# Kernel tuning notes

Hardware: AMD Instinct MI355X
Metric: run time of the kernel (lower is better)

The kernel has to match this reference:

```python
import jax, jax.numpy as jnp
import numpy as np

N_ATOMS = 200000
AEV_DIM = 384
H1, H2, H3 = 160, 128, 96
N_SPECIES = 4
ALPHA = 0.1  # CELU alpha used by ANI atomic networks


def setup_inputs() -> dict:
    key = jax.random.key(0)
    ks = jax.random.split(key, 8)
    aev = jax.random.normal(ks[0], (N_ATOMS, AEV_DIM), dtype=jnp.float32)
    # Disjoint species partition (matches (species==s).nonzero() buffers)
    perm = jax.random.permutation(ks[1], N_ATOMS)
    chunk = N_ATOMS // N_SPECIES
    H_idx = perm[0 * chunk:1 * chunk]
    C_idx = perm[1 * chunk:2 * chunk]
    N_idx = perm[2 * chunk:3 * chunk]
    O_idx = perm[3 * chunk:4 * chunk]

    def init(k, shape, fan_in):
        return (jax.random.normal(k, shape, dtype=jnp.float32) / np.float32(np.sqrt(fan_in)))

    # Stacked per-species MLP params: leading axis = species (H,C,N,O)
    W1 = init(ks[2], (N_SPECIES, AEV_DIM, H1), AEV_DIM); b1 = jnp.zeros((N_SPECIES, H1), jnp.float32)
    W2 = init(ks[3], (N_SPECIES, H1, H2), H1);          b2 = jnp.zeros((N_SPECIES, H2), jnp.float32)
    W3 = init(ks[4], (N_SPECIES, H2, H3), H2);          b3 = jnp.zeros((N_SPECIES, H3), jnp.float32)
    W4 = init(ks[5], (N_SPECIES, H3, 1), H3);           b4 = jnp.zeros((N_SPECIES, 1), jnp.float32)
    return {"aev": aev,
            "W1": W1, "b1": b1, "W2": W2, "b2": b2,
            "W3": W3, "b3": b3, "W4": W4, "b4": b4,
            "H_idx": H_idx, "C_idx": C_idx, "N_idx": N_idx, "O_idx": O_idx}


def _species_mlp(x, W1, b1, W2, b2, W3, b3, W4, b4):
    h = jax.nn.celu(x @ W1 + b1, ALPHA)
    h = jax.nn.celu(h @ W2 + b2, ALPHA)
    h = jax.nn.celu(h @ W3 + b3, ALPHA)
    return (h @ W4 + b4).reshape(-1)  # per-atom scalar energy


def reference(aev, W1, b1, W2, b2, W3, b3, W4, b4, H_idx, C_idx, N_idx, O_idx):
    out = jnp.zeros((aev.shape[0],), dtype=aev.dtype)
    # Fixed small loop over the 4 species networks (structurally distinct experts)
    for s, idx in enumerate((H_idx, C_idx, N_idx, O_idx)):
        e = _species_mlp(aev[idx], W1[s], b1[s], W2[s], b2[s], W3[s], b3[s], W4[s], b4[s])
        out = out.at[idx].add(e)  # index_add_ scatter
    # output.unsqueeze(0).sum(dim=1) -> molecular energy, shape [1]
    return out[None, :].sum(axis=1)
```

## Files before the change

### kernel.cpp

```cpp
#include <hip/hip_runtime.h>

#define DI __device__ __forceinline__

constexpr int AEV = 384;
constexpr int H1N = 160;
constexpr int H2N = 128;
constexpr int H3N = 96;
constexpr int NSP = 4;
constexpr int TM  = 128;
constexpr int SP1 = 168;
constexpr int SP2 = 136;
constexpr int SP3 = 104;

using half8  = __attribute__((ext_vector_type(8))) _Float16;
using half4v = __attribute__((ext_vector_type(4))) _Float16;
using f32x4  = __attribute__((ext_vector_type(4))) float;

__device__ __align__(16) _Float16 g_w1[NSP * H1N * AEV];
__device__ __align__(16) _Float16 g_w2[NSP * H2N * H1N];
__device__ __align__(16) _Float16 g_w3[NSP * H3N * H2N];

DI float celu_f(float x) {
  return fmaxf(x, 0.f) + 0.1f * (exp2f(fminf(x, 0.f) * 14.426950408889634f) - 1.f);
}
DI f32x4 mfma16h(half8 a, half8 b, f32x4 c) {
  return __builtin_amdgcn_mfma_f32_16x16x32_f16(a, b, c, 0, 0, 0);
}
DI half8 cvt8(float4 a, float4 b) {
  half8 t;
  t[0] = (_Float16)a.x; t[1] = (_Float16)a.y; t[2] = (_Float16)a.z; t[3] = (_Float16)a.w;
  t[4] = (_Float16)b.x; t[5] = (_Float16)b.y; t[6] = (_Float16)b.z; t[7] = (_Float16)b.w;
  return t;
}

template <int K, int N>
DI void tp(const float* __restrict__ src, _Float16* dst, int id) {
  constexpr int per = K * N;
  int s = id / per, r = id % per;
  int n = r / K, k = r % K;
  dst[s * per + n * K + k] = (_Float16)src[s * per + k * N + n];
}

__global__ void prep(const float* __restrict__ W1, const float* __restrict__ W2,
                     const float* __restrict__ W3, float* __restrict__ out) {
  int id = blockIdx.x * 256 + threadIdx.x;
  if (id == 0) out[0] = 0.f;
  constexpr int E1 = NSP * AEV * H1N;
  constexpr int E2 = NSP * H1N * H2N;
  constexpr int E3 = NSP * H2N * H3N;
  if (id < E1)                 tp<AEV, H1N>(W1, g_w1, id);
  else if (id < E1 + E2)       tp<H1N, H2N>(W2, g_w2, id - E1);
  else if (id < E1 + E2 + E3)  tp<H2N, H3N>(W3, g_w3, id - E1 - E2);
}

__global__ void __launch_bounds__(256) __attribute__((amdgpu_waves_per_eu(2, 2)))
fused_mlp(const float* __restrict__ aev,
          const float* __restrict__ b1, const float* __restrict__ b2,
          const float* __restrict__ b3,
          const float* __restrict__ W4, const float* __restrict__ pb4,
          const int* __restrict__ i0, const int* __restrict__ i1,
          const int* __restrict__ i2, const int* __restrict__ i3,
          int chunk, float* __restrict__ out) {
  __shared__ __align__(16) _Float16 HB[4 * 32 * (SP1 + SP2)];
  __shared__ float RED[4];

  const int tid  = threadIdx.x;
  const int lane = tid & 63, wav = tid >> 6;
  const int l15  = lane & 15, quad = lane >> 4;
  const int s    = blockIdx.y;
  const int* idx = (s == 0) ? i0 : (s == 1) ? i1 : (s == 2) ? i2 : i3;

  _Float16* H1w = HB + wav * (32 * SP1);
  _Float16* H2w = HB + 4 * (32 * SP1) + wav * (32 * SP2);

  const _Float16* w1 = g_w1 + s * H1N * AEV;
  const _Float16* w2 = g_w2 + s * H2N * H1N;
  const _Float16* w3 = g_w3 + s * H3N * H2N;

  const int abase = (blockIdx.x * 4 + wav) * 32;
  const int a0 = abase + l15, a1 = a0 + 16;
  const int r0 = idx[a0 < chunk ? a0 : (chunk - 1)];
  const int r1 = idx[a1 < chunk ? a1 : (chunk - 1)];
  const float* xr0 = aev + (size_t)r0 * AEV + quad * 8;
  const float* xr1 = aev + (size_t)r1 * AEV + quad * 8;

  f32x4 acc[10][2];
#pragma unroll
  for (int m = 0; m < 10; ++m)
#pragma unroll
    for (int nt = 0; nt < 2; ++nt)
#pragma unroll
      for (int i = 0; i < 4; ++i) acc[m][nt][i] = 0.f;

  float4 xf00, xf01, xf10, xf11;
  xf00 = *(const float4*)(xr0); xf01 = *(const float4*)(xr0 + 4);
  xf10 = *(const float4*)(xr1); xf11 = *(const float4*)(xr1 + 4);

#pragma unroll
  for (int ks = 0; ks < 12; ++ks) {
    half8 bv0 = cvt8(xf00, xf01);
    half8 bv1 = cvt8(xf10, xf11);
    if (ks < 11) {
      xf00 = *(const float4*)(xr0 + (ks + 1) * 32);
      xf01 = *(const float4*)(xr0 + (ks + 1) * 32 + 4);
      xf10 = *(const float4*)(xr1 + (ks + 1) * 32);
      xf11 = *(const float4*)(xr1 + (ks + 1) * 32 + 4);
    }
    const _Float16* pa = w1 + l15 * AEV + ks * 32 + quad * 8;
#pragma unroll
    for (int mt = 0; mt < 10; ++mt) {
      half8 a = *(const half8*)(pa + mt * 16 * AEV);
      acc[mt][0] = mfma16h(a, bv0, acc[mt][0]);
      acc[mt][1] = mfma16h(a, bv1, acc[mt][1]);
    }
  }
#pragma unroll
  for (int mt = 0; mt < 10; ++mt) {
    float4 bb = *(const float4*)(b1 + s * H1N + mt * 16 + quad * 4);
#pragma unroll
    for (int nt = 0; nt < 2; ++nt) {
      int atom = nt * 16 + l15;
      half4v o;
      o[0] = (_Float16)celu_f(acc[mt][nt][0] + bb.x);
      o[1] = (_Float16)celu_f(acc[mt][nt][1] + bb.y);
      o[2] = (_Float16)celu_f(acc[mt][nt][2] + bb.z);
      o[3] = (_Float16)celu_f(acc[mt][nt][3] + bb.w);
      *(half4v*)(H1w + atom * SP1 + mt * 16 + quad * 4) = o;
    }
  }

  {
    f32x4 acc2[8][2];
#pragma unroll
    for (int m = 0; m < 8; ++m)
#pragma unroll
      for (int nt = 0; nt < 2; ++nt)
#pragma unroll
        for (int i = 0; i < 4; ++i) acc2[m][nt][i] = 0.f;
    half8 bb2[5][2];
#pragma unroll
    for (int ks = 0; ks < 5; ++ks)
#pragma unroll
      for (int nt = 0; nt < 2; ++nt)
        bb2[ks][nt] = *(const half8*)(H1w + (nt * 16 + l15) * SP1 + ks * 32 + quad * 8);
#pragma unroll
    for (int mt = 0; mt < 8; ++mt) {
      const _Float16* pa = w2 + (mt * 16 + l15) * H1N + quad * 8;
#pragma unroll
      for (int ks = 0; ks < 5; ++ks) {
        half8 a = *(const half8*)(pa + ks * 32);
        acc2[mt][0] = mfma16h(a, bb2[ks][0], acc2[mt][0]);
        acc2[mt][1] = mfma16h(a, bb2[ks][1], acc2[mt][1]);
      }
    }
#pragma unroll
    for (int mt = 0; mt < 8; ++mt) {
      float4 bb = *(const float4*)(b2 + s * H2N + mt * 16 + quad * 4);
#pragma unroll
      for (int nt = 0; nt < 2; ++nt) {
        int atom = nt * 16 + l15;
        half4v o;
        o[0] = (_Float16)celu_f(acc2[mt][nt][0] + bb.x);
        o[1] = (_Float16)celu_f(acc2[mt][nt][1] + bb.y);
        o[2] = (_Float16)celu_f(acc2[mt][nt][2] + bb.z);
        o[3] = (_Float16)celu_f(acc2[mt][nt][3] + bb.w);
        *(half4v*)(H2w + atom * SP2 + mt * 16 + quad * 4) = o;
      }
    }
  }

  {
    f32x4 acc3[6][2];
#pragma unroll
    for (int m = 0; m < 6; ++m)
#pragma unroll
      for (int nt = 0; nt < 2; ++nt)
#pragma unroll
        for (int i = 0; i < 4; ++i) acc3[m][nt][i] = 0.f;
    half8 bb3[4][2];
#pragma unroll
    for (int ks = 0; ks < 4; ++ks)
#pragma unroll
      for (int nt = 0; nt < 2; ++nt)
        bb3[ks][nt] = *(const half8*)(H2w + (nt * 16 + l15) * SP2 + ks * 32 + quad * 8);
#pragma unroll
    for (int mt = 0; mt < 6; ++mt) {
      const _Float16* pa = w3 + (mt * 16 + l15) * H2N + quad * 8;
#pragma unroll
      for (int ks = 0; ks < 4; ++ks) {
        half8 a = *(const half8*)(pa + ks * 32);
        acc3[mt][0] = mfma16h(a, bb3[ks][0], acc3[mt][0]);
        acc3[mt][1] = mfma16h(a, bb3[ks][1], acc3[mt][1]);
      }
    }
#pragma unroll
    for (int mt = 0; mt < 6; ++mt) {
      float4 bb = *(const float4*)(b3 + s * H3N + mt * 16 + quad * 4);
#pragma unroll
      for (int nt = 0; nt < 2; ++nt) {
        int atom = nt * 16 + l15;
        half4v o;
        o[0] = (_Float16)celu_f(acc3[mt][nt][0] + bb.x);
        o[1] = (_Float16)celu_f(acc3[mt][nt][1] + bb.y);
        o[2] = (_Float16)celu_f(acc3[mt][nt][2] + bb.z);
        o[3] = (_Float16)celu_f(acc3[mt][nt][3] + bb.w);
        *(half4v*)(H1w + atom * SP3 + mt * 16 + quad * 4) = o;
      }
    }
  }

  {
    const int atom = lane >> 1, h = lane & 1;
    const _Float16* h3 = H1w + atom * SP3 + h * 48;
    const float* w4 = W4 + s * H3N + h * 48;
    float e = 0.f;
#pragma unroll
    for (int j = 0; j < 6; ++j) {
      half8 hv = *(const half8*)(h3 + j * 8);
      float4 wa = *(const float4*)(w4 + j * 8);
      float4 wb = *(const float4*)(w4 + j * 8 + 4);
      e += (float)hv[0] * wa.x + (float)hv[1] * wa.y + (float)hv[2] * wa.z + (float)hv[3] * wa.w
         + (float)hv[4] * wb.x + (float)hv[5] * wb.y + (float)hv[6] * wb.z + (float)hv[7] * wb.w;
    }
    e += __shfl_down(e, 1, 64);
    bool valid = (h == 0) && (abase + atom < chunk);
    e = valid ? (e + pb4[s]) : 0.f;
#pragma unroll
    for (int off = 32; off > 0; off >>= 1) e += __shfl_down(e, off, 64);
    if (lane == 0) RED[wav] = e;
  }
  __syncthreads();
  if (tid == 0) atomicAdd(out, RED[0] + RED[1] + RED[2] + RED[3]);
}

extern "C" void kernel_launch(void* const* d_in, const int* in_sizes, int n_in,
                              void* d_out, int out_size, void* d_ws, size_t ws_size,
                              hipStream_t stream) {
  (void)n_in; (void)d_ws; (void)ws_size; (void)out_size;
  const float* aev = (const float*)d_in[0];
  const float* W1  = (const float*)d_in[1];
  const float* b1  = (const float*)d_in[2];
  const float* W2  = (const float*)d_in[3];
  const float* b2  = (const float*)d_in[4];
  const float* W3  = (const float*)d_in[5];
  const float* b3  = (const float*)d_in[6];
  const float* W4  = (const float*)d_in[7];
  const float* b4  = (const float*)d_in[8];
  const int* iH = (const int*)d_in[9];
  const int* iC = (const int*)d_in[10];
  const int* iN = (const int*)d_in[11];
  const int* iO = (const int*)d_in[12];
  const int chunk = in_sizes[9];

  constexpr int TOT = NSP * (AEV * H1N + H1N * H2N + H2N * H3N);
  prep<<<TOT / 256, 256, 0, stream>>>(W1, W2, W3, (float*)d_out);

  const int tiles = (chunk + TM - 1) / TM;
  dim3 grid(tiles, NSP);
  fused_mlp<<<grid, 256, 0, stream>>>(aev, b1, b2, b3, W4, b4,
                                      iH, iC, iN, iO, chunk, (float*)d_out);
}
```

Measured before the change: 582.6 us.

## Split fused MLP into layer-1 and layers-2-4 kernels with LDS-resident weights

Replaces the single fused kernel with two kernels. The first computes layer 1 from gathered AEV rows using W1 staged in shared memory and writes fp16 hidden activations to a global buffer. The second stages W2 and W3 in shared memory and runs layers 2–4 plus the reduction. The aim is to stop re-reading weight fragments from global memory for every tile, which costs an extra global round trip for the H1 activations, large LDS footprints, and 1024-thread blocks that may limit occupancy.

```diff
diff --git a/kernel.cpp b/kernel.cpp
--- a/kernel.cpp
+++ b/kernel.cpp
@@ -7,10 +7,10 @@
 constexpr int H2N = 128;
 constexpr int H3N = 96;
 constexpr int NSP = 4;
-constexpr int TM  = 128;
-constexpr int SP1 = 168;
-constexpr int SP2 = 136;
-constexpr int SP3 = 104;
+constexpr int W1P = 392;
+constexpr int W2P = 168;
+constexpr int W3P = 136;
+constexpr int NMAX = 200000;
 
 using half8  = __attribute__((ext_vector_type(8))) _Float16;
 using half4v = __attribute__((ext_vector_type(4))) _Float16;
@@ -19,6 +19,7 @@
 __device__ __align__(16) _Float16 g_w1[NSP * H1N * AEV];
 __device__ __align__(16) _Float16 g_w2[NSP * H2N * H1N];
 __device__ __align__(16) _Float16 g_w3[NSP * H3N * H2N];
+__device__ __align__(16) _Float16 g_h1[(size_t)NMAX * H1N];
 
 DI float celu_f(float x) {
   return fmaxf(x, 0.f) + 0.1f * (exp2f(fminf(x, 0.f) * 14.426950408889634f) - 1.f);
@@ -53,16 +54,12 @@
   else if (id < E1 + E2 + E3)  tp<H2N, H3N>(W3, g_w3, id - E1 - E2);
 }
 
-__global__ void __launch_bounds__(256) __attribute__((amdgpu_waves_per_eu(2, 2)))
-fused_mlp(const float* __restrict__ aev,
-          const float* __restrict__ b1, const float* __restrict__ b2,
-          const float* __restrict__ b3,
-          const float* __restrict__ W4, const float* __restrict__ pb4,
-          const int* __restrict__ i0, const int* __restrict__ i1,
-          const int* __restrict__ i2, const int* __restrict__ i3,
-          int chunk, float* __restrict__ out) {
-  __shared__ __align__(16) _Float16 HB[4 * 32 * (SP1 + SP2)];
-  __shared__ float RED[4];
+__global__ __launch_bounds__(1024, 4) void layer1_k(
+    const float* __restrict__ aev, const float* __restrict__ b1,
+    const int* __restrict__ i0, const int* __restrict__ i1,
+    const int* __restrict__ i2, const int* __restrict__ i3,
+    int chunk) {
+  __shared__ __align__(16) _Float16 W1s[H1N * W1P];
 
   const int tid  = threadIdx.x;
   const int lane = tid & 63, wav = tid >> 6;
@@ -70,167 +67,174 @@
   const int s    = blockIdx.y;
   const int* idx = (s == 0) ? i0 : (s == 1) ? i1 : (s == 2) ? i2 : i3;
 
-  _Float16* H1w = HB + wav * (32 * SP1);
-  _Float16* H2w = HB + 4 * (32 * SP1) + wav * (32 * SP2);
-
-  const _Float16* w1 = g_w1 + s * H1N * AEV;
-  const _Float16* w2 = g_w2 + s * H2N * H1N;
-  const _Float16* w3 = g_w3 + s * H3N * H2N;
-
-  const int abase = (blockIdx.x * 4 + wav) * 32;
-  const int a0 = abase + l15, a1 = a0 + 16;
-  const int r0 = idx[a0 < chunk ? a0 : (chunk - 1)];
-  const int r1 = idx[a1 < chunk ? a1 : (chunk - 1)];
-  const float* xr0 = aev + (size_t)r0 * AEV + quad * 8;
-  const float* xr1 = aev + (size_t)r1 * AEV + quad * 8;
-
-  f32x4 acc[10][2];
+  const _Float16* wsrc = g_w1 + (size_t)s * H1N * AEV;
+#pragma unroll
+  for (int i = 0; i < 8; ++i) {
+    int c = tid + i * 1024;
+    if (c < H1N * (AEV / 8)) {
+      int n = c / (AEV / 8), kc = c % (AEV / 8);
+      *(half8*)(W1s + n * W1P + kc * 8) = *(const half8*)(wsrc + n * AEV + kc * 8);
+    }
+  }
+  __syncthreads();
+
+  const int a = blockIdx.x * 256 + wav * 16 + l15;
+  const bool valid = (a < chunk);
+  const int r = idx[valid ? a : (chunk - 1)];
+  const float* xr = aev + (size_t)r * AEV + quad * 8;
+
+  f32x4 acc[10];
 #pragma unroll
   for (int m = 0; m < 10; ++m)
 #pragma unroll
-    for (int nt = 0; nt < 2; ++nt)
-#pragma unroll
-      for (int i = 0; i < 4; ++i) acc[m][nt][i] = 0.f;
-
-  float4 xf00, xf01, xf10, xf11;
-  xf00 = *(const float4*)(xr0); xf01 = *(const float4*)(xr0 + 4);
-  xf10 = *(const float4*)(xr1); xf11 = *(const float4*)(xr1 + 4);
-
+    for (int i = 0; i < 4; ++i) acc[m][i] = 0.f;
+
+  float4 xf0 = *(const float4*)(xr), xf1 = *(const float4*)(xr + 4);
 #pragma unroll
   for (int ks = 0; ks < 12; ++ks) {
-    half8 bv0 = cvt8(xf00, xf01);
-    half8 bv1 = cvt8(xf10, xf11);
+    half8 bv = cvt8(xf0, xf1);
     if (ks < 11) {
-      xf00 = *(const float4*)(xr0 + (ks + 1) * 32);
-      xf01 = *(const float4*)(xr0 + (ks + 1) * 32 + 4);
-      xf10 = *(const float4*)(xr1 + (ks + 1) * 32);
-      xf11 = *(const float4*)(xr1 + (ks + 1) * 32 + 4);
-    }
-    const _Float16* pa = w1 + l15 * AEV + ks * 32 + quad * 8;
+      xf0 = *(const float4*)(xr + (ks + 1) * 32);
+      xf1 = *(const float4*)(xr + (ks + 1) * 32 + 4);
+    }
 #pragma unroll
     for (int mt = 0; mt < 10; ++mt) {
-      half8 a = *(const half8*)(pa + mt * 16 * AEV);
-      acc[mt][0] = mfma16h(a, bv0, acc[mt][0]);
-      acc[mt][1] = mfma16h(a, bv1, acc[mt][1]);
-    }
-  }
+      half8 aw = *(const half8*)(W1s + (mt * 16 + l15) * W1P + ks * 32 + quad * 8);
+      acc[mt] = mfma16h(aw, bv, acc[mt]);
+    }
+  }
+  _Float16* hrow = g_h1 + ((size_t)s * chunk + a) * H1N;
 #pragma unroll
   for (int mt = 0; mt < 10; ++mt) {
     float4 bb = *(const float4*)(b1 + s * H1N + mt * 16 + quad * 4);
-#pragma unroll
-    for (int nt = 0; nt < 2; ++nt) {
-      int atom = nt * 16 + l15;
-      half4v o;
-      o[0] = (_Float16)celu_f(acc[mt][nt][0] + bb.x);
-      o[1] = (_Float16)celu_f(acc[mt][nt][1] + bb.y);
-      o[2] = (_Float16)celu_f(acc[mt][nt][2] + bb.z);
-      o[3] = (_Float16)celu_f(acc[mt][nt][3] + bb.w);
-      *(half4v*)(H1w + atom * SP1 + mt * 16 + quad * 4) = o;
-    }
-  }
-
+    half4v o;
+    o[0] = (_Float16)celu_f(acc[mt][0] + bb.x);
+    o[1] = (_Float16)celu_f(acc[mt][1] + bb.y);
+    o[2] = (_Float16)celu_f(acc[mt][2] + bb.z);
+    o[3] = (_Float16)celu_f(acc[mt][3] + bb.w);
+    if (valid) *(half4v*)(hrow + mt * 16 + quad * 4) = o;
+  }
+}
+
+__global__ __launch_bounds__(1024, 4) void layer234_k(
+    const float* __restrict__ b2, const float* __restrict__ b3,
+    const float* __restrict__ W4, const float* __restrict__ pb4,
+    int chunk, float* __restrict__ out) {
+  __shared__ __align__(16) _Float16 W2s[H2N * W2P];
+  __shared__ __align__(16) _Float16 W3s[H3N * W3P];
+  __shared__ __align__(16) _Float16 H2s[16 * 16 * W3P];
+  __shared__ float RED[16];
+
+  const int tid  = threadIdx.x;
+  const int lane = tid & 63, wav = tid >> 6;
+  const int l15  = lane & 15, quad = lane >> 4;
+  const int s    = blockIdx.y;
+
+  const _Float16* w2src = g_w2 + (size_t)s * H2N * H1N;
+  const _Float16* w3src = g_w3 + (size_t)s * H3N * H2N;
+#pragma unroll
+  for (int i = 0; i < 3; ++i) {
+    int c = tid + i * 1024;
+    if (c < H2N * (H1N / 8)) {
+      int n = c / (H1N / 8), kc = c % (H1N / 8);
+      *(half8*)(W2s + n * W2P + kc * 8) = *(const half8*)(w2src + n * H1N + kc * 8);
+    }
+  }
+#pragma unroll
+  for (int i = 0; i < 2; ++i) {
+    int c = tid + i * 1024;
+    if (c < H3N * (H2N / 8)) {
+      int n = c / (H2N / 8), kc = c % (H2N / 8);
+      *(half8*)(W3s + n * W3P + kc * 8) = *(const half8*)(w3src + n * H2N + kc * 8);
+    }
+  }
+  __syncthreads();
+
+  const int a = blockIdx.x * 256 + wav * 16 + l15;
+  const bool valid = (a < chunk);
+  const int ac = valid ? a : (chunk - 1);
+  const _Float16* hrow = g_h1 + ((size_t)s * chunk + ac) * H1N + quad * 8;
+  _Float16* H2w = H2s + wav * (16 * W3P);
+
+  half8 bv2[5];
+#pragma unroll
+  for (int ks = 0; ks < 5; ++ks) bv2[ks] = *(const half8*)(hrow + ks * 32);
+  f32x4 acc2[8];
+#pragma unroll
+  for (int m = 0; m < 8; ++m)
+#pragma unroll
+    for (int i = 0; i < 4; ++i) acc2[m][i] = 0.f;
+#pragma unroll
+  for (int mt = 0; mt < 8; ++mt)
+#pragma unroll
+    for (int ks = 0; ks < 5; ++ks) {
+      half8 aw = *(const half8*)(W2s + (mt * 16 + l15) * W2P + ks * 32 + quad * 8);
+      acc2[mt] = mfma16h(aw, bv2[ks], acc2[mt]);
+    }
+#pragma unroll
+  for (int mt = 0; mt < 8; ++mt) {
+    float4 bb = *(const float4*)(b2 + s * H2N + mt * 16 + quad * 4);
+    half4v o;
+    o[0] = (_Float16)celu_f(acc2[mt][0] + bb.x);
+    o[1] = (_Float16)celu_f(acc2[mt][1] + bb.y);
+    o[2] = (_Float16)celu_f(acc2[mt][2] + bb.z);
+    o[3] = (_Float16)celu_f(acc2[mt][3] + bb.w);
+    *(half4v*)(H2w + l15 * W3P + mt * 16 + quad * 4) = o;
+  }
+
+  half8 bv3[4];
+#pragma unroll
+  for (int ks = 0; ks < 4; ++ks)
+    bv3[ks] = *(const half8*)(H2w + l15 * W3P + ks * 32 + quad * 8);
+  f32x4 acc3[6];
+#pragma unroll
+  for (int m = 0; m < 6; ++m)
+#pragma unroll
+    for (int i = 0; i < 4; ++i) acc3[m][i] = 0.f;
+#pragma unroll
+  for (int mt = 0; mt < 6; ++mt)
+#pragma unroll
+    for (int ks = 0; ks < 4; ++ks) {
+      half8 aw = *(const half8*)(W3s + (mt * 16 + l15) * W3P + ks * 32 + quad * 8);
+      acc3[mt] = mfma16h(aw, bv3[ks], acc3[mt]);
+    }
+#pragma unroll
+  for (int mt = 0; mt < 6; ++mt) {
+    float4 bb = *(const float4*)(b3 + s * H3N + mt * 16 + quad * 4);
+    half4v o;
+    o[0] = (_Float16)celu_f(acc3[mt][0] + bb.x);
+    o[1] = (_Float16)celu_f(acc3[mt][1] + bb.y);
+    o[2] = (_Float16)celu_f(acc3[mt][2] + bb.z);
+    o[3] = (_Float16)celu_f(acc3[mt][3] + bb.w);
+    *(half4v*)(H2w + l15 * W3P + mt * 16 + quad * 4) = o;
+  }
+
+  float e = 0.f;
   {
-    f32x4 acc2[8][2];
-#pragma unroll
-    for (int m = 0; m < 8; ++m)
-#pragma unroll
-      for (int nt = 0; nt < 2; ++nt)
-#pragma unroll
-        for (int i = 0; i < 4; ++i) acc2[m][nt][i] = 0.f;
-    half8 bb2[5][2];
-#pragma unroll
-    for (int ks = 0; ks < 5; ++ks)
-#pragma unroll
-      for (int nt = 0; nt < 2; ++nt)
-        bb2[ks][nt] = *(const half8*)(H1w + (nt * 16 + l15) * SP1 + ks * 32 + quad * 8);
-#pragma unroll
-    for (int mt = 0; mt < 8; ++mt) {
-      const _Float16* pa = w2 + (mt * 16 + l15) * H1N + quad * 8;
-#pragma unroll
-      for (int ks = 0; ks < 5; ++ks) {
-        half8 a = *(const half8*)(pa + ks * 32);
-        acc2[mt][0] = mfma16h(a, bb2[ks][0], acc2[mt][0]);
-        acc2[mt][1] = mfma16h(a, bb2[ks][1], acc2[mt][1]);
-      }
-    }
-#pragma unroll
-    for (int mt = 0; mt < 8; ++mt) {
-      float4 bb = *(const float4*)(b2 + s * H2N + mt * 16 + quad * 4);
-#pragma unroll
-      for (int nt = 0; nt < 2; ++nt) {
-        int atom = nt * 16 + l15;
-        half4v o;
-        o[0] = (_Float16)celu_f(acc2[mt][nt][0] + bb.x);
-        o[1] = (_Float16)celu_f(acc2[mt][nt][1] + bb.y);
-        o[2] = (_Float16)celu_f(acc2[mt][nt][2] + bb.z);
-        o[3] = (_Float16)celu_f(acc2[mt][nt][3] + bb.w);
-        *(half4v*)(H2w + atom * SP2 + mt * 16 + quad * 4) = o;
-      }
-    }
-  }
-
-  {
-    f32x4 acc3[6][2];
-#pragma unroll
-    for (int m = 0; m < 6; ++m)
-#pragma unroll
-      for (int nt = 0; nt < 2; ++nt)
-#pragma unroll
-        for (int i = 0; i < 4; ++i) acc3[m][nt][i] = 0.f;
-    half8 bb3[4][2];
-#pragma unroll
-    for (int ks = 0; ks < 4; ++ks)
-#pragma unroll
-      for (int nt = 0; nt < 2; ++nt)
-        bb3[ks][nt] = *(const half8*)(H2w + (nt * 16 + l15) * SP2 + ks * 32 + quad * 8);
-#pragma unroll
-    for (int mt = 0; mt < 6; ++mt) {
-      const _Float16* pa = w3 + (mt * 16 + l15) * H2N + quad * 8;
-#pragma unroll
-      for (int ks = 0; ks < 4; ++ks) {
-        half8 a = *(const half8*)(pa + ks * 32);
-        acc3[mt][0] = mfma16h(a, bb3[ks][0], acc3[mt][0]);
-        acc3[mt][1] = mfma16h(a, bb3[ks][1], acc3[mt][1]);
-      }
-    }
-#pragma unroll
-    for (int mt = 0; mt < 6; ++mt) {
-      float4 bb = *(const float4*)(b3 + s * H3N + mt * 16 + quad * 4);
-#pragma unroll
-      for (int nt = 0; nt < 2; ++nt) {
-        int atom = nt * 16 + l15;
-        half4v o;
-        o[0] = (_Float16)celu_f(acc3[mt][nt][0] + bb.x);
-        o[1] = (_Float16)celu_f(acc3[mt][nt][1] + bb.y);
-        o[2] = (_Float16)celu_f(acc3[mt][nt][2] + bb.z);
-        o[3] = (_Float16)celu_f(acc3[mt][nt][3] + bb.w);
-        *(half4v*)(H1w + atom * SP3 + mt * 16 + quad * 4) = o;
-      }
-    }
-  }
-
-  {
-    const int atom = lane >> 1, h = lane & 1;
-    const _Float16* h3 = H1w + atom * SP3 + h * 48;
-    const float* w4 = W4 + s * H3N + h * 48;
-    float e = 0.f;
-#pragma unroll
-    for (int j = 0; j < 6; ++j) {
+    const _Float16* h3 = H2w + l15 * W3P + quad * 24;
+    const float* w4 = W4 + s * H3N + quad * 24;
+#pragma unroll
+    for (int j = 0; j < 3; ++j) {
       half8 hv = *(const half8*)(h3 + j * 8);
       float4 wa = *(const float4*)(w4 + j * 8);
       float4 wb = *(const float4*)(w4 + j * 8 + 4);
       e += (float)hv[0] * wa.x + (float)hv[1] * wa.y + (float)hv[2] * wa.z + (float)hv[3] * wa.w
          + (float)hv[4] * wb.x + (float)hv[5] * wb.y + (float)hv[6] * wb.z + (float)hv[7] * wb.w;
     }
-    e += __shfl_down(e, 1, 64);
-    bool valid = (h == 0) && (abase + atom < chunk);
-    e = valid ? (e + pb4[s]) : 0.f;
-#pragma unroll
-    for (int off = 32; off > 0; off >>= 1) e += __shfl_down(e, off, 64);
-    if (lane == 0) RED[wav] = e;
-  }
+  }
+  e += __shfl_xor(e, 16, 64);
+  e += __shfl_xor(e, 32, 64);
+  e = (lane < 16 && valid) ? (e + pb4[s]) : 0.f;
+#pragma unroll
+  for (int off = 8; off > 0; off >>= 1) e += __shfl_xor(e, off, 64);
+  if (lane == 0) RED[wav] = e;
   __syncthreads();
-  if (tid == 0) atomicAdd(out, RED[0] + RED[1] + RED[2] + RED[3]);
+  if (tid == 0) {
+    float t = 0.f;
+#pragma unroll
+    for (int i = 0; i < 16; ++i) t += RED[i];
+    atomicAdd(out, t);
+  }
 }
 
 extern "C" void kernel_launch(void* const* d_in, const int* in_sizes, int n_in,
@@ -255,8 +259,7 @@
   constexpr int TOT = NSP * (AEV * H1N + H1N * H2N + H2N * H3N);
   prep<<<TOT / 256, 256, 0, stream>>>(W1, W2, W3, (float*)d_out);
 
-  const int tiles = (chunk + TM - 1) / TM;
-  dim3 grid(tiles, NSP);
-  fused_mlp<<<grid, 256, 0, stream>>>(aev, b1, b2, b3, W4, b4,
-                                      iH, iC, iN, iO, chunk, (float*)d_out);
-}
+  const int tiles = (chunk + 255) / 256;
+  layer1_k<<<dim3(tiles, NSP), 1024, 0, stream>>>(aev, b1, iH, iC, iN, iO, chunk);
+  layer234_k<<<dim3(tiles, NSP), 1024, 0, stream>>>(b2, b3, W4, b4, chunk, (float*)d_out);
+}
```

Result: faster. 512.1 us (-12.1%).
